# Performance work log

Hardware: AMD Instinct MI355X
Metric: run time of the kernel (lower is better)

Reference implementation:

```python
import jax, jax.numpy as jnp
import numpy as np

D = 2            # stalk dimension d
FD = 3           # final_d = d + 1 (add_lp=True, add_hp=False)
HID = 32         # hidden_channels
N_NODES = 50000
E0 = 200000      # undirected edges; directed edge list has 2*E0 entries (second half reversed)
IN_CH = 128
OUT_CH = 32
N_LAYERS = 2
PSIZE = D * (D + 1) // 2  # cayley param size per edge


def _spectral_normalize(W, iters=20):
    # torch spectral_norm: power iteration with detached u, v; sigma = u^T W v
    u = jnp.full((W.shape[0],), 1.0 / np.sqrt(W.shape[0]), W.dtype)
    def body(_, u):
        v = W.T @ u
        v = v / (jnp.linalg.norm(v) + 1e-12)
        u2 = W @ v
        return u2 / (jnp.linalg.norm(u2) + 1e-12)
    u = jax.lax.fori_loop(0, iters, body, u)
    u = jax.lax.stop_gradient(u)
    v = jax.lax.stop_gradient(W.T @ u)
    v = v / (jnp.linalg.norm(v) + 1e-12)
    return W / (u @ W @ v)


def _cayley(p):
    # p: [E, PSIZE] lower-tri params -> skew A -> orthogonal Q = (I - A)^{-1}(I + A)
    E = p.shape[0]
    r, c = jnp.tril_indices(D)
    M = jnp.zeros((E, D, D), p.dtype).at[:, r, c].set(p)
    A = M - jnp.swapaxes(M, 1, 2)
    I = jnp.eye(D, dtype=p.dtype)
    return jnp.linalg.solve(I[None] - A, I[None] + A)


def setup_inputs() -> dict:
    key = jax.random.key(0)
    ks = jax.random.split(key, 8)
    src = jax.random.randint(ks[0], (E0,), 0, N_NODES)
    dst = jax.random.randint(ks[1], (E0,), 0, N_NODES)
    # symmetric directed edge list; edge j and edge j+E0 are reverses of each other
    edge_index = jnp.concatenate([jnp.stack([src, dst]), jnp.stack([dst, src])], axis=1)
    x = jax.random.normal(ks[2], (N_NODES, IN_CH), jnp.float32)
    s = 0.02
    W1 = jax.random.normal(ks[3], (FD * HID, IN_CH), jnp.float32) * s
    b1 = jnp.zeros((FD * HID,), jnp.float32)
    W2 = jax.random.normal(ks[4], (OUT_CH, FD * HID), jnp.float32) * s
    b2 = jnp.zeros((OUT_CH,), jnp.float32)
    W_left = jnp.tile(jnp.eye(FD, dtype=jnp.float32)[None], (N_LAYERS, 1, 1))  # init eye per torch
    W_right = jax.random.normal(ks[5], (N_LAYERS, HID, HID), jnp.float32) / np.sqrt(HID)
    eps = jnp.zeros((N_LAYERS, FD, 1), jnp.float32)
    W_sheaf = jax.random.normal(ks[6], (N_LAYERS, PSIZE, 2 * FD * HID), jnp.float32) * s
    W_wt = jax.random.normal(ks[7], (N_LAYERS, 1, 2 * FD * HID), jnp.float32) * s
    return {"x": x, "edge_index": edge_index, "W1": W1, "b1": b1, "W2": W2, "b2": b2,
            "W_left": W_left, "W_right": W_right, "eps": eps, "W_sheaf": W_sheaf, "W_wt": W_wt}


def reference(x, edge_index, W1, b1, W2, b2, W_left, W_right, eps, W_sheaf, W_wt):
    N = x.shape[0]
    row, col = edge_index[0], edge_index[1]
    e0 = row.shape[0] // 2
    rev = jnp.concatenate([jnp.arange(e0) + e0, jnp.arange(e0)])  # reverse-edge index
    # lin1 + ELU (dropouts = 0 in eval)
    h = jax.nn.elu(x @ W1.T + b1)                 # [N, FD*HID]
    xc = h.reshape(N * FD, HID)                   # [N*FD, HID]
    x0 = xc
    for layer in range(N_LAYERS):
        # --- sheaf learner + edge weight learner (gather endpoint features) ---
        xn = xc.reshape(N, FD * HID)
        cat = jnp.concatenate([xn[row], xn[col]], axis=-1)   # [2*E0, 2*FD*HID]
        p = jnp.tanh(cat @ W_sheaf[layer].T)                 # sheaf map params [2*E0, PSIZE]
        wdir = jax.nn.sigmoid(cat @ W_wt[layer].T)[:, 0]
        w = wdir * wdir[rev]                                 # symmetric edge weight
        # --- normalized connection (bundle) Laplacian ---
        Q = _cayley(p)                                       # per-edge orthogonal maps
        T = jnp.einsum('eij,eik->ejk', Q, Q[rev])            # transport F_u^T F_v
        w2 = w * w
        deg = jax.ops.segment_sum(w2, row, num_segments=N)
        dinv = jnp.where(deg > 0, jax.lax.rsqrt(jnp.maximum(deg, 1e-30)), 0.0)
        cnorm = w2 * dinv[row] * dinv[col]                   # [2*E0]
        # --- left / right weights (spectral-normalized) ---
        Wl = _spectral_normalize(W_left[layer])
        Wr = _spectral_normalize(W_right[layer])
        y = xc.reshape(N, FD, HID)
        y = jnp.einsum('ef,nfh->neh', Wl, y)                 # mix stalk dims
        y = jnp.einsum('neh,ch->nec', y, Wr)                 # mix channels
        # --- apply block-sparse Laplacian: Lx[u] = x[u] - sum_e c_e B_e x[v] ---
        yv = y[col]                                          # gather  [2*E0, FD, HID]
        tv = jnp.concatenate([jnp.einsum('eij,ejh->eih', T, yv[:, :D]), yv[:, D:]], axis=1)
        agg = jax.ops.segment_sum(cnorm[:, None, None] * tv, row, num_segments=N)
        diag = jnp.where(deg > 0, 1.0, 0.0)[:, None, None]
        z = jax.nn.elu((diag * y - agg).reshape(N * FD, HID))
        # --- epsilon-gated residual ---
        coeff = jnp.tile(1.0 + jnp.tanh(eps[layer]), (N, 1))  # [N*FD, 1]
        x0 = coeff * x0 - z
        xc = x0
    return xc.reshape(N, FD * HID) @ W2.T + b2
```

## Files before the change

### kernel.cpp

```cpp
#include <hip/hip_runtime.h>

#define NN 50000
#define E0 200000
#define E2 400000
#define NGROUPS ((NN + 7) / 8)
#define NCHUNK  ((NN + 255) / 256)
#define NTILES  ((NN + 63) / 64)
#define EB      ((E2 + 255) / 256)

typedef __attribute__((ext_vector_type(8))) short short8;
typedef __attribute__((ext_vector_type(4))) float f32x4;

__device__ __forceinline__ float eluf(float x) { return x > 0.0f ? x : expm1f(x); }
__device__ __forceinline__ float fsig(float x) { return 1.0f / (1.0f + __expf(-x)); }
__device__ __forceinline__ float ftanh(float x) {
    float e = __expf(-2.0f * x);
    return (1.0f - e) / (1.0f + e);
}
__device__ __forceinline__ unsigned rne_bf16(float x) {
    unsigned u = __float_as_uint(x);
    return (u + 0x7fffu + ((u >> 16) & 1u)) >> 16;
}

__device__ __forceinline__ void spectral_block(int l, const float* __restrict__ Wl_in,
                                               const float* __restrict__ Wr_in,
                                               float* __restrict__ Wl_out, float* __restrict__ Wr_out) {
    __shared__ float W[32 * 33];
    __shared__ float sscal;
    int t = threadIdx.x;
    for (int i = t; i < 1024; i += 256) W[(i >> 5) * 33 + (i & 31)] = Wr_in[l * 1024 + i];
    __syncthreads();
    if (t < 32) {
        float u = 0.17677669529663688f;
        for (int it = 0; it < 20; ++it) {
            float v = 0.f;
#pragma unroll 8
            for (int r = 0; r < 32; ++r) v = fmaf(W[r * 33 + t], __shfl(u, r, 32), v);
            float s = v * v;
#pragma unroll
            for (int off = 16; off; off >>= 1) s += __shfl_xor(s, off, 32);
            v *= 1.0f / (sqrtf(s) + 1e-12f);
            float u2 = 0.f;
#pragma unroll 8
            for (int c = 0; c < 32; ++c) u2 = fmaf(W[t * 33 + c], __shfl(v, c, 32), u2);
            s = u2 * u2;
#pragma unroll
            for (int off = 16; off; off >>= 1) s += __shfl_xor(s, off, 32);
            u = u2 * (1.0f / (sqrtf(s) + 1e-12f));
        }
        float v = 0.f;
#pragma unroll 8
        for (int r = 0; r < 32; ++r) v = fmaf(W[r * 33 + t], __shfl(u, r, 32), v);
        float s = v * v;
#pragma unroll
        for (int off = 16; off; off >>= 1) s += __shfl_xor(s, off, 32);
        if (t == 0) sscal = (sqrtf(s) + 1e-12f) / s;
    } else if (t == 64) {
        float M[9];
        for (int i = 0; i < 9; ++i) M[i] = Wl_in[l * 9 + i];
        float u[3] = {0.5773502691896258f, 0.5773502691896258f, 0.5773502691896258f};
        float v[3], u2[3];
        for (int it = 0; it < 20; ++it) {
            float s = 0;
            for (int c = 0; c < 3; ++c) { v[c] = M[c] * u[0] + M[3 + c] * u[1] + M[6 + c] * u[2]; s += v[c] * v[c]; }
            float inv = 1.0f / (sqrtf(s) + 1e-12f);
            for (int c = 0; c < 3; ++c) v[c] *= inv;
            s = 0;
            for (int r = 0; r < 3; ++r) { u2[r] = M[r * 3] * v[0] + M[r * 3 + 1] * v[1] + M[r * 3 + 2] * v[2]; s += u2[r] * u2[r]; }
            inv = 1.0f / (sqrtf(s) + 1e-12f);
            for (int r = 0; r < 3; ++r) u[r] = u2[r] * inv;
        }
        float s = 0;
        for (int c = 0; c < 3; ++c) { v[c] = M[c] * u[0] + M[3 + c] * u[1] + M[6 + c] * u[2]; s += v[c] * v[c]; }
        float inv = (sqrtf(s) + 1e-12f) / s;
        for (int i = 0; i < 9; ++i) Wl_out[l * 9 + i] = M[i] * inv;
    }
    __syncthreads();
    float invs = sscal;
    for (int i = t; i < 1024; i += 256) Wr_out[l * 1024 + i] = W[(i >> 5) * 33 + (i & 31)] * invs;
}

__global__ __launch_bounds__(256) void k_setup(const float* __restrict__ Wl_in, const float* __restrict__ Wr_in,
                                               float* __restrict__ Wl_out, float* __restrict__ Wr_out,
                                               int* __restrict__ cnt, int* __restrict__ fill,
                                               float* __restrict__ deg0, int* __restrict__ gtotal) {
    if (blockIdx.x < 2) {
        spectral_block((int)blockIdx.x, Wl_in, Wr_in, Wl_out, Wr_out);
        return;
    }
    int i = (blockIdx.x - 2) * 256 + threadIdx.x;
    if (i == 0) *gtotal = 0;
    if (i < NN) { cnt[i] = 0; fill[i] = 0; deg0[i] = 0.0f; }
}

template<int K, int N, int NH, bool ELU, bool HIST>
__global__ __launch_bounds__(256) void k_gemm(const float* __restrict__ X,
                                              const float* __restrict__ W,
                                              const float* __restrict__ bias,
                                              float* __restrict__ out,
                                              const int* __restrict__ row, int* __restrict__ cnt) {
    constexpr int KP = K + 8;
    constexpr int NT = NH / 16;
    constexpr int KS = K / 32;
    constexpr int NHALVES = N / NH;
    __shared__ __align__(16) unsigned short whi[NH * KP];
    __shared__ __align__(16) unsigned short wlo[NH * KP];
    int tid = threadIdx.x;
    if (HIST) {
        for (int e = blockIdx.x * 256 + tid; e < E2; e += gridDim.x * 256)
            atomicAdd(&cnt[row[e]], 1);
    }
    const int ch = blockIdx.x % NHALVES;
    const int tstream = blockIdx.x / NHALVES;
    const int nstreams = gridDim.x / NHALVES;
    for (int i = tid; i < NH * K; i += 256) {
        float v = W[ch * NH * K + i];
        int r = i / K, c = i % K;
        unsigned h = rne_bf16(v);
        whi[r * KP + c] = (unsigned short)h;
        wlo[r * KP + c] = (unsigned short)rne_bf16(v - __uint_as_float(h << 16));
    }
    __syncthreads();
    int wave = tid >> 6, lane = tid & 63;
    int quad = lane >> 4, r16 = lane & 15;
    for (int t = tstream; t < NTILES; t += nstreams) {
        long m = (long)t * 64 + wave * 16 + r16;
        long mc = m < NN ? m : (NN - 1);
        const float* xrow = X + mc * K + quad * 8;
        short8 ah[KS], al[KS];
#pragma unroll
        for (int ks = 0; ks < KS; ++ks) {
            const float4* xp = (const float4*)(xrow + ks * 32);
            float4 p0 = xp[0], p1 = xp[1];
            float xv[8] = {p0.x, p0.y, p0.z, p0.w, p1.x, p1.y, p1.z, p1.w};
#pragma unroll
            for (int j = 0; j < 8; ++j) {
                unsigned h = rne_bf16(xv[j]);
                ah[ks][j] = (short)h;
                al[ks][j] = (short)rne_bf16(xv[j] - __uint_as_float(h << 16));
            }
        }
        long mbase = (long)t * 64 + wave * 16 + quad * 4;
#pragma unroll
        for (int tt = 0; tt < NT; ++tt) {
            f32x4 acc = (f32x4){0.f, 0.f, 0.f, 0.f};
#pragma unroll
            for (int ks = 0; ks < KS; ++ks) {
                int ro = (tt * 16 + r16) * KP + ks * 32 + quad * 8;
                short8 bh = *(const short8*)&whi[ro];
                short8 bl = *(const short8*)&wlo[ro];
                acc = __builtin_amdgcn_mfma_f32_16x16x32_bf16(ah[ks], bh, acc, 0, 0, 0);
                acc = __builtin_amdgcn_mfma_f32_16x16x32_bf16(al[ks], bh, acc, 0, 0, 0);
                acc = __builtin_amdgcn_mfma_f32_16x16x32_bf16(ah[ks], bl, acc, 0, 0, 0);
            }
            int coln = ch * NH + tt * 16 + r16;
            float b = bias[coln];
#pragma unroll
            for (int rr = 0; rr < 4; ++rr) {
                long mm = mbase + rr;
                if (mm < NN) {
                    float v = acc[rr] + b;
                    if (ELU) v = eluf(v);
                    out[mm * N + coln] = v;
                }
            }
        }
    }
}

__global__ __launch_bounds__(256) void k_scan(const int* __restrict__ cnt, int* __restrict__ start,
                                              int* __restrict__ gtotal) {
    __shared__ int s[256];
    __shared__ int soff;
    int b = blockIdx.x, t = threadIdx.x;
    int i = b * 256 + t;
    int v = (i < NN) ? cnt[i] : 0;
    s[t] = v;
    __syncthreads();
    for (int off = 1; off < 256; off <<= 1) {
        int add = (t >= off) ? s[t - off] : 0;
        __syncthreads();
        s[t] += add;
        __syncthreads();
    }
    if (t == 255) soff = atomicAdd(gtotal, s[255]);
    __syncthreads();
    if (i < NN) start[i] = s[t] - v + soff;
}

__global__ __launch_bounds__(256) void k_filly8(const float* __restrict__ xc,
                                                const float* __restrict__ Wl, const float* __restrict__ Wr,
                                                const float* __restrict__ Wsh, const float* __restrict__ Wwt,
                                                unsigned* __restrict__ yA, unsigned short* __restrict__ yB,
                                                float4* __restrict__ proj,
                                                const int* __restrict__ row, const int* __restrict__ start,
                                                int* __restrict__ fill, int* __restrict__ eslot) {
    int tid = threadIdx.x;
    if (blockIdx.x >= NGROUPS) {
        int e = (blockIdx.x - NGROUPS) * 256 + tid;
        if (e < E2) {
            int u = row[e];
            eslot[e] = start[u] + atomicAdd(&fill[u], 1);
        }
        return;
    }
    __shared__ float wrs[32 * 33];
    __shared__ float wls[9];
    __shared__ float xcs[8][96];
    __shared__ float ws1[192], wt[192];
    int n0 = blockIdx.x * 8;
    for (int i = tid; i < 1024; i += 256) wrs[(i >> 5) * 33 + (i & 31)] = Wr[i];
    if (tid < 9) wls[tid] = Wl[tid];
    if (tid < 192) {
        ws1[tid] = Wsh[192 + tid];
        wt[tid]  = Wwt[tid];
    }
    for (int i = tid; i < 192; i += 256) {
        int nd = i / 24, of = (i % 24) * 4;
        *(float4*)&xcs[nd][of] = *(const float4*)&xc[(n0 + nd) * 96 + of];
    }
    __syncthreads();
    int node = tid >> 5, c = tid & 31;
    int n = n0 + node;
    float a1 = 0, a2 = 0, a3 = 0, a4 = 0;
#pragma unroll
    for (int j = 0; j < 3; ++j) {
        int k = j * 32 + c;
        float xv = xcs[node][k];
        a1 = fmaf(xv, ws1[k], a1);
        a2 = fmaf(xv, ws1[96 + k], a2);
        a3 = fmaf(xv, wt[k], a3);
        a4 = fmaf(xv, wt[96 + k], a4);
    }
#pragma unroll
    for (int off = 16; off; off >>= 1) {
        a1 += __shfl_xor(a1, off);
        a2 += __shfl_xor(a2, off);
        a3 += __shfl_xor(a3, off);
        a4 += __shfl_xor(a4, off);
    }
    if (c == 0) proj[n] = make_float4(a1, a2, a3, a4);
    {
        float t0 = 0, t1 = 0, t2 = 0;
        const float* wr = &wrs[c * 33];
        const float* xr = xcs[node];
#pragma unroll
        for (int h = 0; h < 32; ++h) {
            float w = wr[h];
            t0 = fmaf(xr[h], w, t0);
            t1 = fmaf(xr[32 + h], w, t1);
            t2 = fmaf(xr[64 + h], w, t2);
        }
        float o0 = wls[0] * t0 + wls[1] * t1 + wls[2] * t2;
        float o1 = wls[3] * t0 + wls[4] * t1 + wls[5] * t2;
        float o2 = wls[6] * t0 + wls[7] * t1 + wls[8] * t2;
        yA[n * 32 + c] = rne_bf16(o0) | (rne_bf16(o1) << 16);
        yB[n * 32 + c] = (unsigned short)rne_bf16(o2);
    }
}

__global__ __launch_bounds__(256) void k_coef(const int* __restrict__ row, const int* __restrict__ col,
                                              const int* __restrict__ eslot,
                                              const float4* __restrict__ proj,
                                              uint2* __restrict__ meta, float* __restrict__ deg) {
    int e = blockIdx.x * 256 + threadIdx.x;
    if (e >= E0) return;
    int u = row[e], v = col[e];
    float4 pu = proj[u], pv = proj[v];
    float a_e = ftanh(pu.x + pv.y);
    float a_r = ftanh(pv.x + pu.y);
    float wd_e = fsig(pu.z + pv.w);
    float wd_r = fsig(pv.z + pu.w);
    float w = wd_e * wd_r;
    float w2 = w * w;
    float ie = 1.0f / (1.0f + a_e * a_e), ir = 1.0f / (1.0f + a_r * a_r);
    float ce = (1.0f - a_e * a_e) * ie, se = 2.0f * a_e * ie;
    float cr = (1.0f - a_r * a_r) * ir, sr = 2.0f * a_r * ir;
    float C = ce * cr + se * sr;
    float S = ce * sr - se * cr;
    unsigned cb = rne_bf16(C), sb = rne_bf16(S), wb = rne_bf16(w2);
    meta[eslot[e]]      = make_uint2(cb | (sb << 16), (unsigned)v | (wb << 16));
    meta[eslot[e + E0]] = make_uint2(cb | ((sb ^ 0x8000u) << 16), (unsigned)u | (wb << 16));
    atomicAdd(&deg[u], w2);
    atomicAdd(&deg[v], w2);
}

__device__ __forceinline__ void gather_accum(int s0, int ec, int c,
                                             const uint2* __restrict__ meta,
                                             const float* __restrict__ deg, float du,
                                             const unsigned* __restrict__ yA,
                                             const unsigned short* __restrict__ yB,
                                             float& acc0, float& acc1, float& acc2) {
    for (int bs = 0; bs < ec; bs += 32) {
        int nb2 = min(32, ec - bs);
        float CC = 0, SS = 0, cnl = 0;
        int vj = 0;
        if (c < nb2) {
            uint2 mt = meta[s0 + bs + c];
            vj = (int)(mt.y & 0xffffu);
            float w2 = __uint_as_float(mt.y & 0xffff0000u);
            float Cv = __uint_as_float(mt.x << 16);
            float Sv = __uint_as_float(mt.x & 0xffff0000u);
            float dv = deg[vj];
            float dvi = dv > 0.0f ? rsqrtf(fmaxf(dv, 1e-30f)) : 0.0f;
            cnl = w2 * du * dvi;
            CC = cnl * Cv;
            SS = cnl * Sv;
        }
        int j4 = nb2 & ~3;
        int j = 0;
        for (; j < j4; j += 4) {
#pragma unroll
            for (int jj = 0; jj < 4; ++jj) {
                float Cj = __shfl(CC, j + jj, 32);
                float Sj = __shfl(SS, j + jj, 32);
                float cj = __shfl(cnl, j + jj, 32);
                int v = __shfl(vj, j + jj, 32);
                unsigned ua = yA[v * 32 + c];
                unsigned ub = (unsigned)yB[v * 32 + c];
                float y0 = __uint_as_float(ua << 16);
                float y1 = __uint_as_float(ua & 0xffff0000u);
                float y2 = __uint_as_float(ub << 16);
                acc0 = fmaf(Cj, y0, acc0);
                acc0 = fmaf(-Sj, y1, acc0);
                acc1 = fmaf(Sj, y0, acc1);
                acc1 = fmaf(Cj, y1, acc1);
                acc2 = fmaf(cj, y2, acc2);
            }
        }
        for (; j < nb2; ++j) {
            float Cj = __shfl(CC, j, 32);
            float Sj = __shfl(SS, j, 32);
            float cj = __shfl(cnl, j, 32);
            int v = __shfl(vj, j, 32);
            unsigned ua = yA[v * 32 + c];
            unsigned ub = (unsigned)yB[v * 32 + c];
            float y0 = __uint_as_float(ua << 16);
            float y1 = __uint_as_float(ua & 0xffff0000u);
            float y2 = __uint_as_float(ub << 16);
            acc0 = fmaf(Cj, y0, acc0);
            acc0 = fmaf(-Sj, y1, acc0);
            acc1 = fmaf(Sj, y0, acc1);
            acc1 = fmaf(Cj, y1, acc1);
            acc2 = fmaf(cj, y2, acc2);
        }
    }
}

__global__ __launch_bounds__(256) void k_gatherY(const int* __restrict__ start,
                                                 const int* __restrict__ cnt,
                                                 const uint2* __restrict__ meta,
                                                 const float* __restrict__ deg0,
                                                 const unsigned* __restrict__ yA0,
                                                 const unsigned short* __restrict__ yB0,
                                                 const float* __restrict__ eps,
                                                 float* __restrict__ xc,
                                                 const float* __restrict__ Wl, const float* __restrict__ Wr,
                                                 const float* __restrict__ Wsh, const float* __restrict__ Wwt,
                                                 unsigned* __restrict__ yA1, unsigned short* __restrict__ yB1,
                                                 float4* __restrict__ proj, float* __restrict__ deg1) {
    __shared__ float wrs[32 * 33];
    __shared__ float wls[9];
    __shared__ float xcs[8][96];
    __shared__ float ws1[192], wt[192];
    int tid = threadIdx.x;
    for (int i = tid; i < 1024; i += 256) wrs[(i >> 5) * 33 + (i & 31)] = Wr[i];
    if (tid < 9) wls[tid] = Wl[tid];
    if (tid < 192) {
        ws1[tid] = Wsh[(1 * 3 + 1) * 192 + tid];
        wt[tid]  = Wwt[1 * 192 + tid];
    }
    __syncthreads();
    int node = tid >> 5, c = tid & 31;
    int n = blockIdx.x * 8 + node;
    int s0 = start[n], ec = cnt[n];
    float dn = deg0[n];
    float du = dn > 0.0f ? rsqrtf(fmaxf(dn, 1e-30f)) : 0.0f;
    float acc0 = 0, acc1 = 0, acc2 = 0;
    gather_accum(s0, ec, c, meta, deg0, du, yA0, yB0, acc0, acc1, acc2);
    float diag = dn > 0.0f ? 1.0f : 0.0f;
    unsigned ua = yA0[n * 32 + c];
    unsigned ub = (unsigned)yB0[n * 32 + c];
    float oy0 = __uint_as_float(ua << 16);
    float oy1 = __uint_as_float(ua & 0xffff0000u);
    float oy2 = __uint_as_float(ub << 16);
    float c0 = 1.0f + tanhf(eps[0]);
    float c1 = 1.0f + tanhf(eps[1]);
    float c2 = 1.0f + tanhf(eps[2]);
    int base = n * 96 + c;
    float nx0 = c0 * xc[base]      - eluf(diag * oy0 - acc0);
    float nx1 = c1 * xc[base + 32] - eluf(diag * oy1 - acc1);
    float nx2 = c2 * xc[base + 64] - eluf(diag * oy2 - acc2);
    xc[base] = nx0; xc[base + 32] = nx1; xc[base + 64] = nx2;
    if (c == 0) deg1[n] = 0.0f;
    xcs[node][c] = nx0; xcs[node][32 + c] = nx1; xcs[node][64 + c] = nx2;
    float a1 = nx0 * ws1[c] + nx1 * ws1[32 + c] + nx2 * ws1[64 + c];
    float a2 = nx0 * ws1[96 + c] + nx1 * ws1[128 + c] + nx2 * ws1[160 + c];
    float a3 = nx0 * wt[c] + nx1 * wt[32 + c] + nx2 * wt[64 + c];
    float a4 = nx0 * wt[96 + c] + nx1 * wt[128 + c] + nx2 * wt[160 + c];
#pragma unroll
    for (int off = 16; off; off >>= 1) {
        a1 += __shfl_xor(a1, off);
        a2 += __shfl_xor(a2, off);
        a3 += __shfl_xor(a3, off);
        a4 += __shfl_xor(a4, off);
    }
    if (c == 0) proj[n] = make_float4(a1, a2, a3, a4);
    {
        float t0 = 0, t1 = 0, t2 = 0;
        const float* wr = &wrs[c * 33];
        const float* xr = xcs[node];
#pragma unroll
        for (int h = 0; h < 32; ++h) {
            float w = wr[h];
            t0 = fmaf(xr[h], w, t0);
            t1 = fmaf(xr[32 + h], w, t1);
            t2 = fmaf(xr[64 + h], w, t2);
        }
        float o0 = wls[0] * t0 + wls[1] * t1 + wls[2] * t2;
        float o1 = wls[3] * t0 + wls[4] * t1 + wls[5] * t2;
        float o2 = wls[6] * t0 + wls[7] * t1 + wls[8] * t2;
        yA1[n * 32 + c] = rne_bf16(o0) | (rne_bf16(o1) << 16);
        yB1[n * 32 + c] = (unsigned short)rne_bf16(o2);
    }
}

__global__ __launch_bounds__(256) void k_gather(const int* __restrict__ start,
                                                const int* __restrict__ cnt,
                                                const uint2* __restrict__ meta,
                                                const float* __restrict__ deg,
                                                const unsigned* __restrict__ yA,
                                                const unsigned short* __restrict__ yB,
                                                const float* __restrict__ eps,
                                                int layer, float* __restrict__ xc) {
    int tid = threadIdx.x;
    int node = tid >> 5, c = tid & 31;
    int n = blockIdx.x * 8 + node;
    if (n >= NN) return;
    int s0 = start[n], ec = cnt[n];
    float dn = deg[n];
    float du = dn > 0.0f ? rsqrtf(fmaxf(dn, 1e-30f)) : 0.0f;
    float acc0 = 0, acc1 = 0, acc2 = 0;
    gather_accum(s0, ec, c, meta, deg, du, yA, yB, acc0, acc1, acc2);
    float diag = dn > 0.0f ? 1.0f : 0.0f;
    unsigned ua = yA[n * 32 + c];
    unsigned ub = (unsigned)yB[n * 32 + c];
    float oy0 = __uint_as_float(ua << 16);
    float oy1 = __uint_as_float(ua & 0xffff0000u);
    float oy2 = __uint_as_float(ub << 16);
    float c0 = 1.0f + tanhf(eps[layer * 3 + 0]);
    float c1 = 1.0f + tanhf(eps[layer * 3 + 1]);
    float c2 = 1.0f + tanhf(eps[layer * 3 + 2]);
    int base = n * 96 + c;
    float z0 = eluf(diag * oy0 - acc0);
    float z1 = eluf(diag * oy1 - acc1);
    float z2 = eluf(diag * oy2 - acc2);
    xc[base]      = c0 * xc[base]      - z0;
    xc[base + 32] = c1 * xc[base + 32] - z1;
    xc[base + 64] = c2 * xc[base + 64] - z2;
}

extern "C" void kernel_launch(void* const* d_in, const int* in_sizes, int n_in,
                              void* d_out, int out_size, void* d_ws, size_t ws_size,
                              hipStream_t stream) {
    const float* x     = (const float*)d_in[0];
    const int*   ei    = (const int*)d_in[1];
    const float* W1    = (const float*)d_in[2];
    const float* b1    = (const float*)d_in[3];
    const float* W2    = (const float*)d_in[4];
    const float* b2    = (const float*)d_in[5];
    const float* Wl    = (const float*)d_in[6];
    const float* Wr    = (const float*)d_in[7];
    const float* eps   = (const float*)d_in[8];
    const float* Wsh   = (const float*)d_in[9];
    const float* Wwt   = (const float*)d_in[10];
    float* out = (float*)d_out;
    const int* row = ei;
    const int* col = ei + E2;

    char* pc = (char*)d_ws;
    float* xc     = (float*)pc;          pc += (size_t)NN * 96 * 4;
    uint2* meta   = (uint2*)pc;          pc += (size_t)E2 * 8;
    unsigned* yA0 = (unsigned*)pc;       pc += (size_t)NN * 32 * 4;
    unsigned* yA1 = (unsigned*)pc;       pc += (size_t)NN * 32 * 4;
    unsigned short* yB0 = (unsigned short*)pc; pc += (size_t)NN * 32 * 2;
    unsigned short* yB1 = (unsigned short*)pc; pc += (size_t)NN * 32 * 2;
    pc = (char*)(((size_t)pc + 15) & ~(size_t)15);
    float4* proj  = (float4*)pc;         pc += (size_t)NN * 16;
    float* deg0   = (float*)pc;          pc += (size_t)NN * 4;
    float* deg1   = (float*)pc;          pc += (size_t)NN * 4;
    float* Wl_n   = (float*)pc;          pc += 32 * 4;
    float* Wr_n   = (float*)pc;          pc += 2048 * 4;
    int* cnt      = (int*)pc;            pc += (size_t)NN * 4;
    int* start    = (int*)pc;            pc += (size_t)NN * 4;
    int* fill     = (int*)pc;            pc += (size_t)NN * 4;
    int* eslot    = (int*)pc;            pc += (size_t)E2 * 4;
    int* gtotal   = (int*)pc;            pc += 4;

    k_setup<<<NCHUNK + 2, 256, 0, stream>>>(Wl, Wr, Wl_n, Wr_n, cnt, fill, deg0, gtotal);
    k_gemm<128, 96, 48, true, true><<<1024, 256, 0, stream>>>(x, W1, b1, xc, row, cnt);
    k_scan<<<NCHUNK, 256, 0, stream>>>(cnt, start, gtotal);
    k_filly8<<<NGROUPS + EB, 256, 0, stream>>>(xc, Wl_n, Wr_n, Wsh, Wwt,
                                               yA0, yB0, proj, row, start, fill, eslot);
    k_coef<<<(E0 + 255) / 256, 256, 0, stream>>>(row, col, eslot, proj, meta, deg0);
    k_gatherY<<<NGROUPS, 256, 0, stream>>>(start, cnt, meta, deg0, yA0, yB0, eps, xc,
                                           Wl_n + 9, Wr_n + 1024, Wsh, Wwt, yA1, yB1, proj, deg1);
    k_coef<<<(E0 + 255) / 256, 256, 0, stream>>>(row, col, eslot, proj, meta, deg1);
    k_gather<<<NGROUPS, 256, 0, stream>>>(start, cnt, meta, deg1, yA1, yB1, eps, 1, xc);
    k_gemm<96, 32, 32, false, false><<<782, 256, 0, stream>>>(xc, W2, b2, out, nullptr, nullptr);
}
```

Baseline: 318.9 us.

## Fuse final layer gather with output projection GEMM

The last-layer gather/residual kernel now keeps the updated node features in shared memory and applies the W2 output projection plus bias directly, replacing the separate final GEMM launch and the xc write-back and re-read. In gatherY, the per-node index and degree loads are moved ahead of the shared-memory weight staging so their latency overlaps the barrier. Each block now stages a 96x32 W2 tile in LDS and does a per-lane 96-term dot product, which raises LDS use and may lower occupancy. The bounds check is dropped, which is safe only because NN is a multiple of 8.

```diff
diff --git a/kernel.cpp b/kernel.cpp
--- a/kernel.cpp
+++ b/kernel.cpp
@@ -364,6 +364,10 @@
     __shared__ float xcs[8][96];
     __shared__ float ws1[192], wt[192];
     int tid = threadIdx.x;
+    int node = tid >> 5, c = tid & 31;
+    int n = blockIdx.x * 8 + node;
+    int s0 = start[n], ec = cnt[n];
+    float dn = deg0[n];
     for (int i = tid; i < 1024; i += 256) wrs[(i >> 5) * 33 + (i & 31)] = Wr[i];
     if (tid < 9) wls[tid] = Wl[tid];
     if (tid < 192) {
@@ -371,10 +375,6 @@
         wt[tid]  = Wwt[1 * 192 + tid];
     }
     __syncthreads();
-    int node = tid >> 5, c = tid & 31;
-    int n = blockIdx.x * 8 + node;
-    int s0 = start[n], ec = cnt[n];
-    float dn = deg0[n];
     float du = dn > 0.0f ? rsqrtf(fmaxf(dn, 1e-30f)) : 0.0f;
     float acc0 = 0, acc1 = 0, acc2 = 0;
     gather_accum(s0, ec, c, meta, deg0, du, yA0, yB0, acc0, acc1, acc2);
@@ -425,20 +425,30 @@
     }
 }
 
-__global__ __launch_bounds__(256) void k_gather(const int* __restrict__ start,
-                                                const int* __restrict__ cnt,
-                                                const uint2* __restrict__ meta,
-                                                const float* __restrict__ deg,
-                                                const unsigned* __restrict__ yA,
-                                                const unsigned short* __restrict__ yB,
-                                                const float* __restrict__ eps,
-                                                int layer, float* __restrict__ xc) {
+__global__ __launch_bounds__(256) void k_gatherF(const int* __restrict__ start,
+                                                 const int* __restrict__ cnt,
+                                                 const uint2* __restrict__ meta,
+                                                 const float* __restrict__ deg,
+                                                 const unsigned* __restrict__ yA,
+                                                 const unsigned short* __restrict__ yB,
+                                                 const float* __restrict__ eps,
+                                                 const float* __restrict__ xc,
+                                                 const float* __restrict__ W2, const float* __restrict__ b2,
+                                                 float* __restrict__ out) {
+    __shared__ float w2t[96 * 32];
+    __shared__ float b2s[32];
+    __shared__ float xcs[8][96];
     int tid = threadIdx.x;
     int node = tid >> 5, c = tid & 31;
     int n = blockIdx.x * 8 + node;
-    if (n >= NN) return;
     int s0 = start[n], ec = cnt[n];
     float dn = deg[n];
+    for (int i = tid; i < 3072; i += 256) {
+        int o = i & 31, f = i >> 5;
+        w2t[i] = W2[o * 96 + f];
+    }
+    if (tid < 32) b2s[tid] = b2[tid];
+    __syncthreads();
     float du = dn > 0.0f ? rsqrtf(fmaxf(dn, 1e-30f)) : 0.0f;
     float acc0 = 0, acc1 = 0, acc2 = 0;
     gather_accum(s0, ec, c, meta, deg, du, yA, yB, acc0, acc1, acc2);
@@ -448,16 +458,19 @@
     float oy0 = __uint_as_float(ua << 16);
     float oy1 = __uint_as_float(ua & 0xffff0000u);
     float oy2 = __uint_as_float(ub << 16);
-    float c0 = 1.0f + tanhf(eps[layer * 3 + 0]);
-    float c1 = 1.0f + tanhf(eps[layer * 3 + 1]);
-    float c2 = 1.0f + tanhf(eps[layer * 3 + 2]);
+    float c0 = 1.0f + tanhf(eps[3]);
+    float c1 = 1.0f + tanhf(eps[4]);
+    float c2 = 1.0f + tanhf(eps[5]);
     int base = n * 96 + c;
-    float z0 = eluf(diag * oy0 - acc0);
-    float z1 = eluf(diag * oy1 - acc1);
-    float z2 = eluf(diag * oy2 - acc2);
-    xc[base]      = c0 * xc[base]      - z0;
-    xc[base + 32] = c1 * xc[base + 32] - z1;
-    xc[base + 64] = c2 * xc[base + 64] - z2;
+    float nx0 = c0 * xc[base]      - eluf(diag * oy0 - acc0);
+    float nx1 = c1 * xc[base + 32] - eluf(diag * oy1 - acc1);
+    float nx2 = c2 * xc[base + 64] - eluf(diag * oy2 - acc2);
+    xcs[node][c] = nx0; xcs[node][32 + c] = nx1; xcs[node][64 + c] = nx2;
+    float acc = 0.f;
+    const float* xr = xcs[node];
+#pragma unroll 4
+    for (int f = 0; f < 96; ++f) acc = fmaf(xr[f], w2t[f * 32 + c], acc);
+    out[n * 32 + c] = acc + b2s[c];
 }
 
 extern "C" void kernel_launch(void* const* d_in, const int* in_sizes, int n_in,
@@ -506,6 +519,6 @@
     k_gatherY<<<NGROUPS, 256, 0, stream>>>(start, cnt, meta, deg0, yA0, yB0, eps, xc,
                                            Wl_n + 9, Wr_n + 1024, Wsh, Wwt, yA1, yB1, proj, deg1);
     k_coef<<<(E0 + 255) / 256, 256, 0, stream>>>(row, col, eslot, proj, meta, deg1);
-    k_gather<<<NGROUPS, 256, 0, stream>>>(start, cnt, meta, deg1, yA1, yB1, eps, 1, xc);
-    k_gemm<96, 32, 32, false, false><<<782, 256, 0, stream>>>(xc, W2, b2, out, nullptr, nullptr);
-}
+    k_gatherF<<<NGROUPS, 256, 0, stream>>>(start, cnt, meta, deg1, yA1, yB1, eps, xc,
+                                           W2, b2, out);
+}
```

After: 342.3 us. +7.3%, slower.
